# Kernel optimization log

Hardware: AMD Instinct MI355X
Metric: run time of the kernel (lower is better)

Reference implementation:

```python
import jax, jax.numpy as jnp
import numpy as np

B, S, D = 4, 2048, 1024
NH, HD = 16, 64  # num_heads, head_dim; NH*HD == D


def setup_inputs() -> dict:
    key = jax.random.key(0)
    ks = jax.random.split(key, 10)
    s = 0.02
    return {
        "x": jax.random.normal(ks[0], (B, S, D), dtype=jnp.float32),
        "attention_mask": jnp.zeros((B, 1, 1, S), dtype=jnp.float32),
        "Wq": jax.random.normal(ks[1], (D, D), dtype=jnp.float32) * s,
        "bq": jnp.zeros((D,), dtype=jnp.float32),
        "Wk": jax.random.normal(ks[2], (D, D), dtype=jnp.float32) * s,
        "bk": jnp.zeros((D,), dtype=jnp.float32),
        "Wv": jax.random.normal(ks[3], (D, D), dtype=jnp.float32) * s,
        "bv": jnp.zeros((D,), dtype=jnp.float32),
        "Wo": jax.random.normal(ks[4], (D, D), dtype=jnp.float32) * s,
        "bo": jnp.zeros((D,), dtype=jnp.float32),
    }


def _heads(t):
    # [B,S,D] -> [B,NH,S,HD]
    return t.reshape(B, S, NH, HD).transpose(0, 2, 1, 3)


def reference(x, attention_mask, Wq, bq, Wk, bk, Wv, bv, Wo, bo):
    q = _heads(x @ Wq + bq)
    k = _heads(x @ Wk + bk)
    v = _heads(x @ Wv + bv)
    scores = jnp.einsum("bhqd,bhkd->bhqk", q, k) / jnp.sqrt(jnp.float32(HD))
    scores = scores + attention_mask
    attn = jax.nn.softmax(scores, axis=-1)  # dropout p=0 -> identity
    ctx = jnp.einsum("bhqk,bhkd->bhqd", attn, v)
    ctx = ctx.transpose(0, 2, 1, 3).reshape(B, S, D)
    return ctx @ Wo + bo
```

## Files before the change

### kernel.cpp

```cpp
#include <hip/hip_runtime.h>
#include <cstdint>
#include <cstddef>

typedef unsigned short u16;
typedef __attribute__((ext_vector_type(8))) __bf16 bf16x8;
typedef __attribute__((ext_vector_type(4))) float f32x4;
typedef __attribute__((ext_vector_type(16))) float f32x16;
typedef __attribute__((ext_vector_type(2))) uint32_t u32x2;
typedef __attribute__((ext_vector_type(4))) float float4v;

#define BATCH 4
#define S_LEN 2048
#define DMODEL 1024
#define NHEAD 16
#define HDIM 64
#define MROWS (BATCH * S_LEN)
#define LOG2E 1.4426950408889634f
#define SC_L (0.125f * LOG2E)

__device__ __forceinline__ u16 f2bf(float f) {
  uint32_t u = __float_as_uint(f);
  u += 0x7fffu + ((u >> 16) & 1u);
  return (u16)(u >> 16);
}

#if __has_builtin(__builtin_amdgcn_cvt_pk_bf16_f32)
__device__ __forceinline__ uint32_t packbf2(float a, float b) {
  auto t = __builtin_amdgcn_cvt_pk_bf16_f32(a, b);
  uint32_t u;
  __builtin_memcpy(&u, &t, 4);
  return u;
}
#else
__device__ __forceinline__ uint32_t packbf2(float a, float b) {
  uint32_t ua = __float_as_uint(a) + 0x8000u;
  uint32_t ub = __float_as_uint(b) + 0x8000u;
  return (ub & 0xFFFF0000u) | (ua >> 16);
}
#endif

#if __has_builtin(__builtin_amdgcn_exp2f)
#define EXP2(x) __builtin_amdgcn_exp2f(x)
#else
#define EXP2(x) exp2f(x)
#endif

typedef __attribute__((address_space(1))) void gvoid_t;
typedef __attribute__((address_space(3))) void svoid_t;
__device__ __forceinline__ void gl_lds16(const void* g, void* s) {
  __builtin_amdgcn_global_load_lds((gvoid_t*)g, (svoid_t*)s, 16, 0, 0);
}

__global__ __launch_bounds__(256) void cvt4_kernel(const float4v* __restrict__ in,
                                                   u32x2* __restrict__ out, int n4) {
  int i = blockIdx.x * blockDim.x + threadIdx.x;
  if (i < n4) {
    float4v v = in[i];
    u32x2 o;
    o.x = packbf2(v.x, v.y);
    o.y = packbf2(v.z, v.w);
    out[i] = o;
  }
}

__global__ __launch_bounds__(256) void maskl_kernel(const float* __restrict__ in,
                                                    float* __restrict__ out, int n) {
  int i = blockIdx.x * blockDim.x + threadIdx.x;
  if (i < n) out[i] = in[i] * LOG2E;
}

__global__ __launch_bounds__(256) void tcvt_kernel(const float* __restrict__ W0,
                                                   const float* __restrict__ W1,
                                                   const float* __restrict__ W2,
                                                   const float* __restrict__ W3,
                                                   u16* __restrict__ Wall) {
  __shared__ float tile[32][33];
  const int z = blockIdx.z;
  const float* W = (z == 0) ? W0 : (z == 1) ? W1 : (z == 2) ? W2 : W3;
  u16* Wt = Wall + (size_t)z * DMODEL * DMODEL;
  const int n0 = blockIdx.x * 32, k0 = blockIdx.y * 32;
  const int x = threadIdx.x, y = threadIdx.y;
  for (int yy = y; yy < 32; yy += 8)
    tile[yy][x] = W[(size_t)(k0 + yy) * DMODEL + n0 + x];
  __syncthreads();
  for (int yy = y; yy < 32; yy += 8)
    Wt[(size_t)(n0 + yy) * DMODEL + k0 + x] = f2bf(tile[x][yy]);
}

template <int MODE>
__global__ __launch_bounds__(256) void gemm128(const u16* __restrict__ A,
                                               const u16* __restrict__ Bt,
                                               const float* __restrict__ b0,
                                               const float* __restrict__ b1,
                                               const float* __restrict__ b2,
                                               void* __restrict__ o0,
                                               void* __restrict__ o1,
                                               void* __restrict__ o2) {
  __shared__ u16 As[128 * 32];
  __shared__ u16 Bs[128 * 32];
  const int tid = threadIdx.x;
  const int wid = tid >> 6;
  const int lane = tid & 63;
  const int l16 = lane & 15;
  const int g4 = lane >> 4;
  const int nwg = gridDim.x * gridDim.y;
  int flat = blockIdx.y * gridDim.x + blockIdx.x;
  flat = (flat & 7) * (nwg >> 3) + (flat >> 3);
  const int m0 = (flat & 63) * 128;
  const int n0 = (flat >> 6) * 128;
  const int wm = (wid & 1) * 64;
  const int wn = (wid >> 1) * 64;

  const int srow = tid >> 2;
  const int sk = (tid & 3) * 8;
  const u16* gA = A + (size_t)(m0 + srow) * DMODEL + sk;
  const u16* gB = Bt + (size_t)(n0 + srow) * DMODEL + sk;
  char* sA = (char*)As + wid * 1024;
  char* sB = (char*)Bs + wid * 1024;

  f32x4 acc[4][4];
#pragma unroll
  for (int i = 0; i < 4; ++i)
#pragma unroll
    for (int j = 0; j < 4; ++j) acc[i][j] = (f32x4){0.f, 0.f, 0.f, 0.f};

  for (int k0 = 0; k0 < DMODEL; k0 += 32) {
    __syncthreads();
    gl_lds16(gA + k0, sA);
    gl_lds16(gA + (size_t)64 * DMODEL + k0, sA + 4096);
    gl_lds16(gB + k0, sB);
    gl_lds16(gB + (size_t)64 * DMODEL + k0, sB + 4096);
    __syncthreads();

    bf16x8 af[4], bfr[4];
#pragma unroll
    for (int i = 0; i < 4; ++i)
      af[i] = *(const bf16x8*)(As + (wm + i * 16 + l16) * 32 + g4 * 8);
#pragma unroll
    for (int j = 0; j < 4; ++j)
      bfr[j] = *(const bf16x8*)(Bs + (wn + j * 16 + l16) * 32 + g4 * 8);
#pragma unroll
    for (int i = 0; i < 4; ++i)
#pragma unroll
      for (int j = 0; j < 4; ++j)
        acc[i][j] = __builtin_amdgcn_mfma_f32_16x16x32_bf16(af[i], bfr[j],
                                                            acc[i][j], 0, 0, 0);
  }

  const int seg = n0 >> 10;
  const float* bp = (MODE == 1 || seg == 0) ? b0 : (seg == 1 ? b1 : b2);
  void* op = (MODE == 1 || seg == 0) ? o0 : (seg == 1 ? o1 : o2);

#pragma unroll
  for (int i = 0; i < 4; ++i) {
#pragma unroll
    for (int j = 0; j < 4; ++j) {
      const int coll = n0 + wn + j * 16 + l16;
      const int cseg = coll & 1023;
      const float bval = bp[cseg];
#pragma unroll
      for (int r = 0; r < 4; ++r) {
        const int rowg = m0 + wm + i * 16 + g4 * 4 + r;
        const float v = acc[i][j][r] + bval;
        if (MODE == 0) {
          const int b = rowg >> 11, s = rowg & (S_LEN - 1);
          const int h = cseg >> 6, d = cseg & (HDIM - 1);
          if (seg == 2) {
            ((u16*)op)[(((size_t)(b * NHEAD + h) * HDIM + d) << 11) + s] = f2bf(v);
          } else {
            ((u16*)op)[((size_t)((b * NHEAD + h) * S_LEN + s) << 6) + d] = f2bf(v);
          }
        } else {
          ((float*)op)[(size_t)rowg * DMODEL + cseg] = v;
        }
      }
    }
  }
}

__global__ __launch_bounds__(256, 2) void attn4_kernel(const u16* __restrict__ Q,
                                                       const u16* __restrict__ K,
                                                       const u16* __restrict__ Vt,
                                                       const float* __restrict__ maskL,
                                                       u16* __restrict__ ctx) {
  __shared__ u16 Ks[2][64 * 72];
  __shared__ u16 Vs[2][64 * 72];

  const int tid = threadIdx.x;
  const int wid = tid >> 6;
  const int lane = tid & 63;
  const int l32 = lane & 31;
  const int hi = lane >> 5;
  const int flat = blockIdx.y * gridDim.x + blockIdx.x;
  const int nf = (flat & 7) * 64 + (flat >> 3);
  const int bx = nf & 7;
  const int bh = nf >> 3;
  const int b = bh >> 4;
  const int h = bh & 15;
  const int qw0 = bx * 256 + wid * 64;

  const u16* Qbase = Q + (size_t)bh * S_LEN * HDIM;
  bf16x8 aq[2][4];
#pragma unroll
  for (int qh = 0; qh < 2; ++qh)
#pragma unroll
    for (int c = 0; c < 4; ++c)
      aq[qh][c] = *(const bf16x8*)(Qbase + (size_t)(qw0 + qh * 32 + l32) * HDIM +
                                   c * 16 + hi * 8);

  union { u16 s[8]; bf16x8 v; } onesu;
#pragma unroll
  for (int i = 0; i < 8; ++i) onesu.s[i] = 0x3F80;
  const bf16x8 onesv = onesu.v;

  const f32x16 z16 = {};
  f32x16 oacc[2][2] = {};
  f32x16 lacc[2] = {};

  const int srow = tid >> 3;
  const int scol = (tid & 7) * 8;
  const int keyg = scol >> 4;
  const int todd = (scol >> 3) & 1;
  const int vkb = keyg * 16 + todd * 4;
  const u16* Kg = K + (size_t)bh * S_LEN * HDIM + (size_t)srow * HDIM + scol;
  const u16* Vg = Vt + (size_t)bh * HDIM * S_LEN + (size_t)srow * S_LEN + scol;
  const float* mrow = maskL + (size_t)b * S_LEN;

  bf16x8 kv0, kv1;
  union VU { bf16x8 v; uint32_t u[4]; };
  VU vv0, vv1;

  auto LOADT = [&](int kt) {
    kv0 = *(const bf16x8*)(Kg + (size_t)kt * HDIM);
    kv1 = *(const bf16x8*)(Kg + (size_t)(kt + 32) * HDIM);
    vv0.v = *(const bf16x8*)(Vg + kt);
    vv1.v = *(const bf16x8*)(Vg + (size_t)32 * S_LEN + kt);
  };
  auto STORET = [&](int buf) {
    u16* Kb = &Ks[buf][0];
    u16* Vb = &Vs[buf][0];
    *(bf16x8*)(Kb + srow * 72 + scol) = kv0;
    *(bf16x8*)(Kb + (srow + 32) * 72 + scol) = kv1;
    *(u32x2*)(Vb + srow * 72 + vkb) = (u32x2){vv0.u[0], vv0.u[1]};
    *(u32x2*)(Vb + srow * 72 + vkb + 8) = (u32x2){vv0.u[2], vv0.u[3]};
    *(u32x2*)(Vb + (srow + 32) * 72 + vkb) = (u32x2){vv1.u[0], vv1.u[1]};
    *(u32x2*)(Vb + (srow + 32) * 72 + vkb + 8) = (u32x2){vv1.u[2], vv1.u[3]};
  };

  auto COMPUTE = [&](int buf, int kt) {
    const u16* Kb = &Ks[buf][0];
    const u16* Vb = &Vs[buf][0];
    uint32_t P[2][2][8];
#pragma unroll
    for (int T = 0; T < 2; ++T) {
      bf16x8 kf[4];
#pragma unroll
      for (int c = 0; c < 4; ++c)
        kf[c] = *(const bf16x8*)(Kb + (T * 32 + l32) * 72 + c * 16 + hi * 8);
      f32x4 m4[4];
#pragma unroll
      for (int tq = 0; tq < 4; ++tq)
        m4[tq] = *(const f32x4*)(mrow + kt + T * 32 + tq * 8 + hi * 4);
#pragma unroll
      for (int qh = 0; qh < 2; ++qh) {
        __builtin_amdgcn_s_setprio(1);
        f32x16 s = __builtin_amdgcn_mfma_f32_32x32x16_bf16(kf[0], aq[qh][0], z16, 0, 0, 0);
#pragma unroll
        for (int c = 1; c < 4; ++c)
          s = __builtin_amdgcn_mfma_f32_32x32x16_bf16(kf[c], aq[qh][c], s, 0, 0, 0);
        __builtin_amdgcn_s_setprio(0);
#pragma unroll
        for (int tq = 0; tq < 4; ++tq) {
          float p0 = EXP2(fmaf(s[tq * 4 + 0], SC_L, m4[tq][0]));
          float p1 = EXP2(fmaf(s[tq * 4 + 1], SC_L, m4[tq][1]));
          float p2 = EXP2(fmaf(s[tq * 4 + 2], SC_L, m4[tq][2]));
          float p3 = EXP2(fmaf(s[tq * 4 + 3], SC_L, m4[tq][3]));
          P[T][qh][tq * 2] = packbf2(p0, p1);
          P[T][qh][tq * 2 + 1] = packbf2(p2, p3);
        }
      }
    }

#pragma unroll
    for (int c = 0; c < 4; ++c) {
      const int T = c >> 1, half = c & 1;
      bf16x8 vf[2];
#pragma unroll
      for (int dh = 0; dh < 2; ++dh)
        vf[dh] = *(const bf16x8*)(Vb + (dh * 32 + l32) * 72 + c * 16 + hi * 8);
      __builtin_amdgcn_s_setprio(1);
#pragma unroll
      for (int qh = 0; qh < 2; ++qh) {
        union { uint32_t u[4]; bf16x8 v; } pf;
#pragma unroll
        for (int e = 0; e < 4; ++e) pf.u[e] = P[T][qh][half * 4 + e];
        oacc[qh][0] = __builtin_amdgcn_mfma_f32_32x32x16_bf16(pf.v, vf[0], oacc[qh][0], 0, 0, 0);
        oacc[qh][1] = __builtin_amdgcn_mfma_f32_32x32x16_bf16(pf.v, vf[1], oacc[qh][1], 0, 0, 0);
        lacc[qh] = __builtin_amdgcn_mfma_f32_32x32x16_bf16(pf.v, onesv, lacc[qh], 0, 0, 0);
      }
      __builtin_amdgcn_s_setprio(0);
    }
  };

  LOADT(0);
  STORET(0);
  __syncthreads();
  int cur = 0;
  for (int kt = 0; kt < S_LEN - 64; kt += 64) {
    LOADT(kt + 64);
    COMPUTE(cur, kt);
    STORET(cur ^ 1);
    __syncthreads();
    cur ^= 1;
  }
  COMPUTE(cur, S_LEN - 64);

#pragma unroll
  for (int qh = 0; qh < 2; ++qh) {
#pragma unroll
    for (int reg = 0; reg < 16; ++reg) {
      const int q = qw0 + qh * 32 + (reg & 3) + 8 * (reg >> 2) + 4 * hi;
      const float inv = 1.0f / lacc[qh][reg];
      u16* cp = ctx + ((size_t)(b * S_LEN + q) * NHEAD + h) * HDIM;
      cp[l32] = f2bf(oacc[qh][0][reg] * inv);
      cp[32 + l32] = f2bf(oacc[qh][1][reg] * inv);
    }
  }
}

extern "C" void kernel_launch(void* const* d_in, const int* in_sizes, int n_in,
                              void* d_out, int out_size, void* d_ws, size_t ws_size,
                              hipStream_t stream) {
  const float* x = (const float*)d_in[0];
  const float* mask = (const float*)d_in[1];
  const float* Wq = (const float*)d_in[2];
  const float* bq = (const float*)d_in[3];
  const float* Wk = (const float*)d_in[4];
  const float* bk = (const float*)d_in[5];
  const float* Wv = (const float*)d_in[6];
  const float* bv = (const float*)d_in[7];
  const float* Wo = (const float*)d_in[8];
  const float* bo = (const float*)d_in[9];
  float* out = (float*)d_out;

  char* ws = (char*)d_ws;
  size_t off = 0;
  u16* xb = (u16*)(ws + off);    off += (size_t)MROWS * DMODEL * 2;
  u16* wall = (u16*)(ws + off);  off += (size_t)4 * DMODEL * DMODEL * 2;
  u16* Qh = (u16*)(ws + off);    off += (size_t)MROWS * DMODEL * 2;
  u16* Kh = (u16*)(ws + off);    off += (size_t)MROWS * DMODEL * 2;
  u16* Vtb = (u16*)(ws + off);   off += (size_t)MROWS * DMODEL * 2;
  u16* ctxb = (u16*)(ws + off);  off += (size_t)MROWS * DMODEL * 2;
  float* mL = (float*)(ws + off); off += (size_t)BATCH * S_LEN * 4;
  (void)ws_size; (void)in_sizes; (void)n_in; (void)out_size;

  const int nx4 = MROWS * DMODEL / 4;
  cvt4_kernel<<<dim3(nx4 / 256), dim3(256), 0, stream>>>((const float4v*)x, (u32x2*)xb, nx4);
  maskl_kernel<<<dim3(BATCH * S_LEN / 256), dim3(256), 0, stream>>>(mask, mL, BATCH * S_LEN);
  tcvt_kernel<<<dim3(32, 32, 4), dim3(32, 8), 0, stream>>>(Wq, Wk, Wv, Wo, wall);

  gemm128<0><<<dim3(MROWS / 128, 3 * DMODEL / 128), dim3(256), 0, stream>>>(
      xb, wall, bq, bk, bv, (void*)Qh, (void*)Kh, (void*)Vtb);

  attn4_kernel<<<dim3(S_LEN / 256, BATCH * NHEAD), dim3(256), 0, stream>>>(Qh, Kh, Vtb, mL, ctxb);

  gemm128<1><<<dim3(MROWS / 128, DMODEL / 128), dim3(256), 0, stream>>>(
      ctxb, wall + (size_t)3 * DMODEL * DMODEL, bo, bo, bo, (void*)out, (void*)out, (void*)out);
}
```

Baseline: 325.5 us.

## Halve attention query tile per wave and raise occupancy; drop GEMM block swizzle

The attention kernel now gives each wave 32 query rows instead of 64, so each block covers 128 queries and the grid doubles. Launch bounds rise to 4 blocks per CU, which cuts register pressure (fewer accumulators and P fragments) and allows more latency hiding. In exchange each K/V tile loaded into shared memory is reused by half as many queries, doubling K/V traffic. Separately, the GEMM drops its XCD-aware block remapping in favour of a plain blockIdx mapping, which may change L2 locality.

```diff
diff --git a/kernel.cpp b/kernel.cpp
--- a/kernel.cpp
+++ b/kernel.cpp
@@ -103,11 +103,8 @@
   const int lane = tid & 63;
   const int l16 = lane & 15;
   const int g4 = lane >> 4;
-  const int nwg = gridDim.x * gridDim.y;
-  int flat = blockIdx.y * gridDim.x + blockIdx.x;
-  flat = (flat & 7) * (nwg >> 3) + (flat >> 3);
-  const int m0 = (flat & 63) * 128;
-  const int n0 = (flat >> 6) * 128;
+  const int m0 = blockIdx.x * 128;
+  const int n0 = blockIdx.y * 128;
   const int wm = (wid & 1) * 64;
   const int wn = (wid >> 1) * 64;
 
@@ -178,7 +175,7 @@
   }
 }
 
-__global__ __launch_bounds__(256, 2) void attn4_kernel(const u16* __restrict__ Q,
+__global__ __launch_bounds__(256, 4) void attn6_kernel(const u16* __restrict__ Q,
                                                        const u16* __restrict__ K,
                                                        const u16* __restrict__ Vt,
                                                        const float* __restrict__ maskL,
@@ -192,21 +189,18 @@
   const int l32 = lane & 31;
   const int hi = lane >> 5;
   const int flat = blockIdx.y * gridDim.x + blockIdx.x;
-  const int nf = (flat & 7) * 64 + (flat >> 3);
-  const int bx = nf & 7;
-  const int bh = nf >> 3;
+  const int nf = (flat & 7) * 128 + (flat >> 3);
+  const int bx = nf & 15;
+  const int bh = nf >> 4;
   const int b = bh >> 4;
   const int h = bh & 15;
-  const int qw0 = bx * 256 + wid * 64;
+  const int qw0 = bx * 128 + wid * 32;
 
   const u16* Qbase = Q + (size_t)bh * S_LEN * HDIM;
-  bf16x8 aq[2][4];
-#pragma unroll
-  for (int qh = 0; qh < 2; ++qh)
-#pragma unroll
-    for (int c = 0; c < 4; ++c)
-      aq[qh][c] = *(const bf16x8*)(Qbase + (size_t)(qw0 + qh * 32 + l32) * HDIM +
-                                   c * 16 + hi * 8);
+  bf16x8 aq[4];
+#pragma unroll
+  for (int c = 0; c < 4; ++c)
+    aq[c] = *(const bf16x8*)(Qbase + (size_t)(qw0 + l32) * HDIM + c * 16 + hi * 8);
 
   union { u16 s[8]; bf16x8 v; } onesu;
 #pragma unroll
@@ -214,8 +208,8 @@
   const bf16x8 onesv = onesu.v;
 
   const f32x16 z16 = {};
-  f32x16 oacc[2][2] = {};
-  f32x16 lacc[2] = {};
+  f32x16 oacc[2] = {};
+  f32x16 lacc = {};
 
   const int srow = tid >> 3;
   const int scol = (tid & 7) * 8;
@@ -250,7 +244,7 @@
   auto COMPUTE = [&](int buf, int kt) {
     const u16* Kb = &Ks[buf][0];
     const u16* Vb = &Vs[buf][0];
-    uint32_t P[2][2][8];
+    uint32_t P[2][8];
 #pragma unroll
     for (int T = 0; T < 2; ++T) {
       bf16x8 kf[4];
@@ -261,23 +255,20 @@
 #pragma unroll
       for (int tq = 0; tq < 4; ++tq)
         m4[tq] = *(const f32x4*)(mrow + kt + T * 32 + tq * 8 + hi * 4);
-#pragma unroll
-      for (int qh = 0; qh < 2; ++qh) {
-        __builtin_amdgcn_s_setprio(1);
-        f32x16 s = __builtin_amdgcn_mfma_f32_32x32x16_bf16(kf[0], aq[qh][0], z16, 0, 0, 0);
-#pragma unroll
-        for (int c = 1; c < 4; ++c)
-          s = __builtin_amdgcn_mfma_f32_32x32x16_bf16(kf[c], aq[qh][c], s, 0, 0, 0);
-        __builtin_amdgcn_s_setprio(0);
-#pragma unroll
-        for (int tq = 0; tq < 4; ++tq) {
-          float p0 = EXP2(fmaf(s[tq * 4 + 0], SC_L, m4[tq][0]));
-          float p1 = EXP2(fmaf(s[tq * 4 + 1], SC_L, m4[tq][1]));
-          float p2 = EXP2(fmaf(s[tq * 4 + 2], SC_L, m4[tq][2]));
-          float p3 = EXP2(fmaf(s[tq * 4 + 3], SC_L, m4[tq][3]));
-          P[T][qh][tq * 2] = packbf2(p0, p1);
-          P[T][qh][tq * 2 + 1] = packbf2(p2, p3);
-        }
+      __builtin_amdgcn_s_setprio(1);
+      f32x16 s = __builtin_amdgcn_mfma_f32_32x32x16_bf16(kf[0], aq[0], z16, 0, 0, 0);
+#pragma unroll
+      for (int c = 1; c < 4; ++c)
+        s = __builtin_amdgcn_mfma_f32_32x32x16_bf16(kf[c], aq[c], s, 0, 0, 0);
+      __builtin_amdgcn_s_setprio(0);
+#pragma unroll
+      for (int tq = 0; tq < 4; ++tq) {
+        float p0 = EXP2(fmaf(s[tq * 4 + 0], SC_L, m4[tq][0]));
+        float p1 = EXP2(fmaf(s[tq * 4 + 1], SC_L, m4[tq][1]));
+        float p2 = EXP2(fmaf(s[tq * 4 + 2], SC_L, m4[tq][2]));
+        float p3 = EXP2(fmaf(s[tq * 4 + 3], SC_L, m4[tq][3]));
+        P[T][tq * 2] = packbf2(p0, p1);
+        P[T][tq * 2 + 1] = packbf2(p2, p3);
       }
     }
 
@@ -288,16 +279,13 @@
 #pragma unroll
       for (int dh = 0; dh < 2; ++dh)
         vf[dh] = *(const bf16x8*)(Vb + (dh * 32 + l32) * 72 + c * 16 + hi * 8);
+      union { uint32_t u[4]; bf16x8 v; } pf;
+#pragma unroll
+      for (int e = 0; e < 4; ++e) pf.u[e] = P[T][half * 4 + e];
       __builtin_amdgcn_s_setprio(1);
-#pragma unroll
-      for (int qh = 0; qh < 2; ++qh) {
-        union { uint32_t u[4]; bf16x8 v; } pf;
-#pragma unroll
-        for (int e = 0; e < 4; ++e) pf.u[e] = P[T][qh][half * 4 + e];
-        oacc[qh][0] = __builtin_amdgcn_mfma_f32_32x32x16_bf16(pf.v, vf[0], oacc[qh][0], 0, 0, 0);
-        oacc[qh][1] = __builtin_amdgcn_mfma_f32_32x32x16_bf16(pf.v, vf[1], oacc[qh][1], 0, 0, 0);
-        lacc[qh] = __builtin_amdgcn_mfma_f32_32x32x16_bf16(pf.v, onesv, lacc[qh], 0, 0, 0);
-      }
+      oacc[0] = __builtin_amdgcn_mfma_f32_32x32x16_bf16(pf.v, vf[0], oacc[0], 0, 0, 0);
+      oacc[1] = __builtin_amdgcn_mfma_f32_32x32x16_bf16(pf.v, vf[1], oacc[1], 0, 0, 0);
+      lacc = __builtin_amdgcn_mfma_f32_32x32x16_bf16(pf.v, onesv, lacc, 0, 0, 0);
       __builtin_amdgcn_s_setprio(0);
     }
   };
@@ -316,15 +304,12 @@
   COMPUTE(cur, S_LEN - 64);
 
 #pragma unroll
-  for (int qh = 0; qh < 2; ++qh) {
-#pragma unroll
-    for (int reg = 0; reg < 16; ++reg) {
-      const int q = qw0 + qh * 32 + (reg & 3) + 8 * (reg >> 2) + 4 * hi;
-      const float inv = 1.0f / lacc[qh][reg];
-      u16* cp = ctx + ((size_t)(b * S_LEN + q) * NHEAD + h) * HDIM;
-      cp[l32] = f2bf(oacc[qh][0][reg] * inv);
-      cp[32 + l32] = f2bf(oacc[qh][1][reg] * inv);
-    }
+  for (int reg = 0; reg < 16; ++reg) {
+    const int q = qw0 + (reg & 3) + 8 * (reg >> 2) + 4 * hi;
+    const float inv = 1.0f / lacc[reg];
+    u16* cp = ctx + ((size_t)(b * S_LEN + q) * NHEAD + h) * HDIM;
+    cp[l32] = f2bf(oacc[0][reg] * inv);
+    cp[32 + l32] = f2bf(oacc[1][reg] * inv);
   }
 }
 
@@ -362,7 +347,7 @@
   gemm128<0><<<dim3(MROWS / 128, 3 * DMODEL / 128), dim3(256), 0, stream>>>(
       xb, wall, bq, bk, bv, (void*)Qh, (void*)Kh, (void*)Vtb);
 
-  attn4_kernel<<<dim3(S_LEN / 256, BATCH * NHEAD), dim3(256), 0, stream>>>(Qh, Kh, Vtb, mL, ctxb);
+  attn6_kernel<<<dim3(S_LEN / 128, BATCH * NHEAD), dim3(256), 0, stream>>>(Qh, Kh, Vtb, mL, ctxb);
 
   gemm128<1><<<dim3(MROWS / 128, DMODEL / 128), dim3(256), 0, stream>>>(
       ctxb, wall + (size_t)3 * DMODEL * DMODEL, bo, bo, bo, (void*)out, (void*)out, (void*)out);
```

Measured after the change: 475.0 us. 46.0% more time.
